# Kernel tuning notes

Hardware: AMD Instinct MI355X
Metric: run time of the kernel (lower is better)

Reference implementation:

```python
import jax, jax.numpy as jnp
import numpy as np


def setup_inputs() -> dict:
    key = jax.random.key(0)
    x = jax.random.normal(key, (32, 1, 1024, 1024), dtype=jnp.float32)
    return {"x": x}


def reference(x) -> jnp.ndarray:
    # Original torch loop computes a running max down the height dim (dim=2)
    # for channel 0 (C=1 here), overwriting each element with the prefix max.
    # This is exactly a cumulative-max (prefix-max scan) along axis=2.
    return jax.lax.associative_scan(jnp.maximum, x, axis=2)
```

## Files before the change

kernel.cpp:

```cpp
#include <hip/hip_runtime.h>


constexpr int B = 32;
constexpr int H = 1024;
constexpr int W = 1024;
constexpr int ROW4 = W / 4;
constexpr int NSEG = 32;
constexpr int SH = H / NSEG;
constexpr int NB = B * NSEG;
constexpr size_t TOT_BYTES = (size_t)NB * ROW4 * sizeof(float4);

__device__ __forceinline__ float4 max4(float4 a, float4 b) {
    return make_float4(fmaxf(a.x, b.x), fmaxf(a.y, b.y),
                       fmaxf(a.z, b.z), fmaxf(a.w, b.w));
}

__global__ __launch_bounds__(256) void seg_colmax(const float* __restrict__ xf,
                                                  float* __restrict__ tf) {
    const int id = blockIdx.x;
    const int b = id >> 5;
    const int s = id & (NSEG - 1);
    const int t = threadIdx.x;
    const float4* x4 = (const float4*)xf;
    float4* t4 = (float4*)tf;

    const size_t base = ((size_t)b * H + (size_t)s * SH) * ROW4 + t;
    const float ninf = -__builtin_inff();
    float4 m = make_float4(ninf, ninf, ninf, ninf);

#pragma unroll
    for (int g = 0; g < SH; g += 8) {
        float4 v[8];
#pragma unroll
        for (int r = 0; r < 8; ++r) v[r] = x4[base + (size_t)(g + r) * ROW4];
#pragma unroll
        for (int r = 0; r < 8; ++r) m = max4(m, v[r]);
    }
    t4[(size_t)id * ROW4 + t] = m;
}

__global__ __launch_bounds__(256) void seg_apply(const float* __restrict__ xf,
                                                 const float* __restrict__ tf,
                                                 float* __restrict__ of) {
    const int id0 = blockIdx.x;
    const int id = (id0 & 7) * (NB / 8) + (id0 >> 3);
    const int b = id >> 5;
    const int s = id & (NSEG - 1);
    const int t = threadIdx.x;
    const float4* x4 = (const float4*)xf;
    const float4* t4 = (const float4*)tf;
    float4* o4 = (float4*)of;

    const float ninf = -__builtin_inff();
    float4 carry = make_float4(ninf, ninf, ninf, ninf);

#pragma unroll
    for (int g = 0; g < NSEG; g += 8) {
        float4 v[8];
#pragma unroll
        for (int k = 0; k < 8; ++k)
            v[k] = t4[(size_t)(b * NSEG + g + k) * ROW4 + t];
#pragma unroll
        for (int k = 0; k < 8; ++k)
            if (g + k < s) carry = max4(carry, v[k]);
    }

    const size_t base = ((size_t)b * H + (size_t)s * SH) * ROW4 + t;
    float4 m = carry;
#pragma unroll
    for (int g = 0; g < SH; g += 8) {
        float4 v[8];
#pragma unroll
        for (int r = 0; r < 8; ++r) v[r] = x4[base + (size_t)(g + r) * ROW4];
#pragma unroll
        for (int r = 0; r < 8; ++r) {
            m = max4(m, v[r]);
            o4[base + (size_t)(g + r) * ROW4] = m;
        }
    }
}

constexpr int F_SW4 = 8;
constexpr int F_NSTRIP = ROW4 / F_SW4;
constexpr int F_CH = 128;
constexpr int F_NCHUNK = H / F_CH;
constexpr int F_R = 4;

__device__ __forceinline__ float4 shflup4(float4 v, int d) {
    float4 r;
    r.x = __shfl_up(v.x, d, 64);
    r.y = __shfl_up(v.y, d, 64);
    r.z = __shfl_up(v.z, d, 64);
    r.w = __shfl_up(v.w, d, 64);
    return r;
}

__global__ __launch_bounds__(256) void cummax_sp(const float* __restrict__ xf,
                                                 float* __restrict__ of) {
    __shared__ float4 wavetot[2][32];
    const int tid = threadIdx.x;
    const int lane = tid & 63;
    const int wid = tid >> 6;
    const int w = tid & 7;
    const int hsegG = tid >> 3;
    const int hseg_l = (tid >> 3) & 7;
    const int b = blockIdx.x >> 5;
    const int strip = blockIdx.x & (F_NSTRIP - 1);
    const float4* x4 = (const float4*)xf;
    float4* o4 = (float4*)of;
    const size_t tbase = (size_t)b * (H * ROW4) + (size_t)strip * F_SW4 + w;
    const float ninf = -__builtin_inff();
    const float4 ninf4 = make_float4(ninf, ninf, ninf, ninf);
    float4 carry = ninf4;
    float4 cur[F_R], nxt[F_R];
#pragma unroll
    for (int r = 0; r < F_R; ++r)
        cur[r] = x4[tbase + (size_t)(hsegG * F_R + r) * ROW4];
#pragma unroll
    for (int c = 0; c < F_NCHUNK; ++c) {
        if (c + 1 < F_NCHUNK) {
#pragma unroll
            for (int r = 0; r < F_R; ++r)
                nxt[r] = x4[tbase + (size_t)((c + 1) * F_CH + hsegG * F_R + r) * ROW4];
        }
        float4 m = max4(max4(cur[0], cur[1]), max4(cur[2], cur[3]));
        float4 incl = m;
        { float4 t = shflup4(incl, 8);  if (lane >= 8)  incl = max4(incl, t); }
        { float4 t = shflup4(incl, 16); if (lane >= 16) incl = max4(incl, t); }
        { float4 t = shflup4(incl, 32); if (lane >= 32) incl = max4(incl, t); }
        float4 ew = shflup4(incl, 8);
        float4 excl = (hseg_l == 0) ? ninf4 : ew;
        if (hseg_l == 7) wavetot[c & 1][wid * 8 + w] = incl;
        __syncthreads();
        float4 crosspre = carry;
        float4 tot = carry;
#pragma unroll
        for (int w2 = 0; w2 < 4; ++w2) {
            float4 v = wavetot[c & 1][w2 * 8 + w];
            if (w2 < wid) crosspre = max4(crosspre, v);
            tot = max4(tot, v);
        }
        carry = tot;
        float4 a = max4(crosspre, excl);
#pragma unroll
        for (int r = 0; r < F_R; ++r) {
            a = max4(a, cur[r]);
            o4[tbase + (size_t)(c * F_CH + hsegG * F_R + r) * ROW4] = a;
        }
        if (c + 1 < F_NCHUNK) {
#pragma unroll
            for (int r = 0; r < F_R; ++r) cur[r] = nxt[r];
        }
    }
}

extern "C" void kernel_launch(void* const* d_in, const int* in_sizes, int n_in,
                              void* d_out, int out_size, void* d_ws, size_t ws_size,
                              hipStream_t stream) {
    const float* x = (const float*)d_in[0];
    float* out = (float*)d_out;
    if (ws_size >= TOT_BYTES && d_ws != nullptr) {
        float* tot = (float*)d_ws;
        seg_colmax<<<NB, 256, 0, stream>>>(x, tot);
        seg_apply<<<NB, 256, 0, stream>>>(x, tot, out);
    } else {
        cummax_sp<<<B * F_NSTRIP, 256, 0, stream>>>(x, out);
    }
}
```

Before: 259.3 us.

## Fuse two-pass segmented cummax into single kernel with inter-block flag handoff

Replaces the separate column-max and apply kernels with one kernel. Each block publishes its segment aggregate and sets a release flag, then waits on the flags of preceding segments in the same batch before applying the carry. If a wait times out, the block recomputes that segment's max from the input, so it never deadlocks. This removes a kernel launch boundary and lets the second read of x hit cache soon after the first. In exchange it adds a memset, spin-waiting on flags, and possible redundant reads when blocks are not co-resident.

```diff
diff --git a/kernel.cpp b/kernel.cpp
--- a/kernel.cpp
+++ b/kernel.cpp
@@ -8,26 +8,30 @@
 constexpr int NSEG = 32;
 constexpr int SH = H / NSEG;
 constexpr int NB = B * NSEG;
-constexpr size_t TOT_BYTES = (size_t)NB * ROW4 * sizeof(float4);
+constexpr size_t AGG_BYTES = (size_t)NB * ROW4 * sizeof(float4);
+constexpr size_t WS_BYTES = AGG_BYTES + (size_t)NB * sizeof(unsigned);
 
 __device__ __forceinline__ float4 max4(float4 a, float4 b) {
     return make_float4(fmaxf(a.x, b.x), fmaxf(a.y, b.y),
                        fmaxf(a.z, b.z), fmaxf(a.w, b.w));
 }
 
-__global__ __launch_bounds__(256) void seg_colmax(const float* __restrict__ xf,
-                                                  float* __restrict__ tf) {
+__global__ __launch_bounds__(256) void cummax_lb(const float* __restrict__ xf,
+                                                 float* __restrict__ of,
+                                                 float4* __restrict__ agg,
+                                                 unsigned* __restrict__ flags) {
     const int id = blockIdx.x;
     const int b = id >> 5;
     const int s = id & (NSEG - 1);
     const int t = threadIdx.x;
     const float4* x4 = (const float4*)xf;
-    float4* t4 = (float4*)tf;
+    float4* o4 = (float4*)of;
+    const size_t base = ((size_t)b * H + (size_t)s * SH) * ROW4 + t;
 
-    const size_t base = ((size_t)b * H + (size_t)s * SH) * ROW4 + t;
     const float ninf = -__builtin_inff();
-    float4 m = make_float4(ninf, ninf, ninf, ninf);
+    const float4 ninf4 = make_float4(ninf, ninf, ninf, ninf);
 
+    float4 m = ninf4;
 #pragma unroll
     for (int g = 0; g < SH; g += 8) {
         float4 v[8];
@@ -36,37 +40,42 @@
 #pragma unroll
         for (int r = 0; r < 8; ++r) m = max4(m, v[r]);
     }
-    t4[(size_t)id * ROW4 + t] = m;
-}
+    agg[(size_t)id * ROW4 + t] = m;
+    __syncthreads();
+    if (t == 0)
+        __hip_atomic_store(&flags[id], 1u, __ATOMIC_RELEASE,
+                           __HIP_MEMORY_SCOPE_AGENT);
 
-__global__ __launch_bounds__(256) void seg_apply(const float* __restrict__ xf,
-                                                 const float* __restrict__ tf,
-                                                 float* __restrict__ of) {
-    const int id0 = blockIdx.x;
-    const int id = (id0 & 7) * (NB / 8) + (id0 >> 3);
-    const int b = id >> 5;
-    const int s = id & (NSEG - 1);
-    const int t = threadIdx.x;
-    const float4* x4 = (const float4*)xf;
-    const float4* t4 = (const float4*)tf;
-    float4* o4 = (float4*)of;
+    __shared__ unsigned missing_sh;
+    if (t == 0) {
+        unsigned miss = 0;
+        for (int k = 0; k < s; ++k) {
+            int tries = 0;
+            while (__hip_atomic_load(&flags[(id & ~(NSEG - 1)) | k],
+                                     __ATOMIC_ACQUIRE,
+                                     __HIP_MEMORY_SCOPE_AGENT) == 0u) {
+                if (++tries > (1 << 15)) { miss |= 1u << k; break; }
+                __builtin_amdgcn_s_sleep(2);
+            }
+        }
+        missing_sh = miss;
+    }
+    __syncthreads();
+    const unsigned miss = missing_sh;
 
-    const float ninf = -__builtin_inff();
-    float4 carry = make_float4(ninf, ninf, ninf, ninf);
-
-#pragma unroll
-    for (int g = 0; g < NSEG; g += 8) {
-        float4 v[8];
-#pragma unroll
-        for (int k = 0; k < 8; ++k)
-            v[k] = t4[(size_t)(b * NSEG + g + k) * ROW4 + t];
-#pragma unroll
-        for (int k = 0; k < 8; ++k)
-            if (g + k < s) carry = max4(carry, v[k]);
+    float4 carry = ninf4;
+    for (int k = 0; k < s; ++k) {
+        if ((miss >> k) & 1u) {
+            const size_t kb = ((size_t)b * H + (size_t)k * SH) * ROW4 + t;
+            float4 a = ninf4;
+            for (int r = 0; r < SH; ++r)
+                a = max4(a, x4[kb + (size_t)r * ROW4]);
+            carry = max4(carry, a);
+        } else {
+            carry = max4(carry, agg[(size_t)((id & ~(NSEG - 1)) | k) * ROW4 + t]);
+        }
     }
 
-    const size_t base = ((size_t)b * H + (size_t)s * SH) * ROW4 + t;
-    float4 m = carry;
 #pragma unroll
     for (int g = 0; g < SH; g += 8) {
         float4 v[8];
@@ -74,8 +83,8 @@
         for (int r = 0; r < 8; ++r) v[r] = x4[base + (size_t)(g + r) * ROW4];
 #pragma unroll
         for (int r = 0; r < 8; ++r) {
-            m = max4(m, v[r]);
-            o4[base + (size_t)(g + r) * ROW4] = m;
+            carry = max4(carry, v[r]);
+            o4[base + (size_t)(g + r) * ROW4] = carry;
         }
     }
 }
@@ -159,10 +168,11 @@
                               hipStream_t stream) {
     const float* x = (const float*)d_in[0];
     float* out = (float*)d_out;
-    if (ws_size >= TOT_BYTES && d_ws != nullptr) {
-        float* tot = (float*)d_ws;
-        seg_colmax<<<NB, 256, 0, stream>>>(x, tot);
-        seg_apply<<<NB, 256, 0, stream>>>(x, tot, out);
+    if (d_ws != nullptr && ws_size >= WS_BYTES) {
+        float4* agg = (float4*)d_ws;
+        unsigned* flags = (unsigned*)((char*)d_ws + AGG_BYTES);
+        hipMemsetAsync(flags, 0, NB * sizeof(unsigned), stream);
+        cummax_lb<<<NB, 256, 0, stream>>>(x, out, agg, flags);
     } else {
         cummax_sp<<<B * F_NSTRIP, 256, 0, stream>>>(x, out);
     }
```

Result: slower. 469.5 us (+81.1%).

## Fuse segment reduce and apply into one cooperative kernel with grid sync

Applied to the files above, without the earlier changes.

Merges the two-pass segmented scan (segment column-max, then carry-and-apply) into a single cooperative kernel that uses a grid-wide barrier between phases. Each block keeps its segment in flight across the barrier and re-reads x after the sync. The carry loop now runs only up to the block's segment index instead of over all segments. It removes one kernel launch, but every block must be co-resident (1024 blocks of 256 threads) and pays for the grid barrier; if the cooperative launch fails, it falls back to the single-pass kernel.

```diff
diff --git a/kernel.cpp b/kernel.cpp
--- a/kernel.cpp
+++ b/kernel.cpp
@@ -1,4 +1,7 @@
 #include <hip/hip_runtime.h>
+#include <hip/hip_cooperative_groups.h>
+
+namespace cg = cooperative_groups;
 
 
 constexpr int B = 32;
@@ -8,26 +11,29 @@
 constexpr int NSEG = 32;
 constexpr int SH = H / NSEG;
 constexpr int NB = B * NSEG;
-constexpr size_t TOT_BYTES = (size_t)NB * ROW4 * sizeof(float4);
+constexpr size_t AGG_BYTES = (size_t)NB * ROW4 * sizeof(float4);
 
 __device__ __forceinline__ float4 max4(float4 a, float4 b) {
     return make_float4(fmaxf(a.x, b.x), fmaxf(a.y, b.y),
                        fmaxf(a.z, b.z), fmaxf(a.w, b.w));
 }
 
-__global__ __launch_bounds__(256) void seg_colmax(const float* __restrict__ xf,
-                                                  float* __restrict__ tf) {
+__global__ __launch_bounds__(256, 4) void cummax_coop(const float* __restrict__ xf,
+                                                      float* __restrict__ of,
+                                                      float* __restrict__ aggf) {
     const int id = blockIdx.x;
     const int b = id >> 5;
     const int s = id & (NSEG - 1);
     const int t = threadIdx.x;
     const float4* x4 = (const float4*)xf;
-    float4* t4 = (float4*)tf;
+    float4* o4 = (float4*)of;
+    float4* agg = (float4*)aggf;
+    const size_t base = ((size_t)b * H + (size_t)s * SH) * ROW4 + t;
 
-    const size_t base = ((size_t)b * H + (size_t)s * SH) * ROW4 + t;
     const float ninf = -__builtin_inff();
-    float4 m = make_float4(ninf, ninf, ninf, ninf);
+    const float4 ninf4 = make_float4(ninf, ninf, ninf, ninf);
 
+    float4 m = ninf4;
 #pragma unroll
     for (int g = 0; g < SH; g += 8) {
         float4 v[8];
@@ -36,37 +42,21 @@
 #pragma unroll
         for (int r = 0; r < 8; ++r) m = max4(m, v[r]);
     }
-    t4[(size_t)id * ROW4 + t] = m;
-}
+    agg[(size_t)id * ROW4 + t] = m;
 
-__global__ __launch_bounds__(256) void seg_apply(const float* __restrict__ xf,
-                                                 const float* __restrict__ tf,
-                                                 float* __restrict__ of) {
-    const int id0 = blockIdx.x;
-    const int id = (id0 & 7) * (NB / 8) + (id0 >> 3);
-    const int b = id >> 5;
-    const int s = id & (NSEG - 1);
-    const int t = threadIdx.x;
-    const float4* x4 = (const float4*)xf;
-    const float4* t4 = (const float4*)tf;
-    float4* o4 = (float4*)of;
+    cg::this_grid().sync();
 
-    const float ninf = -__builtin_inff();
-    float4 carry = make_float4(ninf, ninf, ninf, ninf);
-
-#pragma unroll
-    for (int g = 0; g < NSEG; g += 8) {
+    float4 carry = ninf4;
+    for (int g = 0; g < s; g += 8) {
         float4 v[8];
 #pragma unroll
         for (int k = 0; k < 8; ++k)
-            v[k] = t4[(size_t)(b * NSEG + g + k) * ROW4 + t];
+            v[k] = agg[(size_t)(b * NSEG + g + k) * ROW4 + t];
 #pragma unroll
         for (int k = 0; k < 8; ++k)
             if (g + k < s) carry = max4(carry, v[k]);
     }
 
-    const size_t base = ((size_t)b * H + (size_t)s * SH) * ROW4 + t;
-    float4 m = carry;
 #pragma unroll
     for (int g = 0; g < SH; g += 8) {
         float4 v[8];
@@ -74,8 +64,8 @@
         for (int r = 0; r < 8; ++r) v[r] = x4[base + (size_t)(g + r) * ROW4];
 #pragma unroll
         for (int r = 0; r < 8; ++r) {
-            m = max4(m, v[r]);
-            o4[base + (size_t)(g + r) * ROW4] = m;
+            carry = max4(carry, v[r]);
+            o4[base + (size_t)(g + r) * ROW4] = carry;
         }
     }
 }
@@ -159,11 +149,14 @@
                               hipStream_t stream) {
     const float* x = (const float*)d_in[0];
     float* out = (float*)d_out;
-    if (ws_size >= TOT_BYTES && d_ws != nullptr) {
-        float* tot = (float*)d_ws;
-        seg_colmax<<<NB, 256, 0, stream>>>(x, tot);
-        seg_apply<<<NB, 256, 0, stream>>>(x, tot, out);
-    } else {
-        cummax_sp<<<B * F_NSTRIP, 256, 0, stream>>>(x, out);
+    if (d_ws != nullptr && ws_size >= AGG_BYTES) {
+        float* agg = (float*)d_ws;
+        void* args[3] = {(void*)&x, (void*)&out, (void*)&agg};
+        hipError_t e = hipLaunchCooperativeKernel(
+            reinterpret_cast<const void*>(cummax_coop), dim3(NB), dim3(256),
+            args, 0, stream);
+        if (e == hipSuccess) return;
+        (void)hipGetLastError();
     }
+    cummax_sp<<<B * F_NSTRIP, 256, 0, stream>>>(x, out);
 }
```

Result: slower. 375.6 us (+44.9%).
